# Kernel tuning notes

Hardware: AMD Instinct MI355X
Metric: run time of the kernel (lower is better)

The kernel has to match this reference:

```python
import jax, jax.numpy as jnp
import numpy as np

N, D, F, M, K = 4096, 1024, 4096, 2048, 307
EPS = 1e-5

def _ln(h, g, b):
    mu = jnp.mean(h, axis=-1, keepdims=True)
    var = jnp.mean(jnp.square(h - mu), axis=-1, keepdims=True)
    return (h - mu) * jax.lax.rsqrt(var + EPS) * g + b

def _attn(h, wq, wk, wv, mask):
    # wq/wk/wv stored as [D, D] so y = h @ w matches torch Linear(h) with W.T
    q = h @ wq
    k = h @ wk
    v = h @ wv
    s = (q @ k.T) * (1.0 / np.sqrt(D))  # [N, N]
    s = jnp.where(mask, -1e9, s)
    a = jax.nn.softmax(s, axis=-1)
    return a @ v, a

def _ffn(h, w1, b1, w2, b2):
    return jax.nn.gelu(h @ w1 + b1, approximate=False) @ w2 + b2

def setup_inputs() -> dict:
    ks = jax.random.split(jax.random.key(0), 32)
    s = 0.02
    p = lambda i, shape: (jax.random.normal(ks[i], shape, jnp.float32) * s)
    inp = {
        'x': jax.random.normal(ks[0], (N, D), jnp.float32),
        'real_edge_mask': jax.random.bernoulli(ks[1], 0.5, (N, N)),
        'fake_edge_mask': jax.random.bernoulli(ks[2], 0.5, (N, N)),
        'mask_nodes': jax.random.permutation(ks[3], N)[:M].astype(jnp.int32),
        'gene_idx': jnp.argsort(jax.random.uniform(ks[4], (M, D)), axis=-1)[:, :K].astype(jnp.int32),
        'wq1': p(5, (D, D)), 'wk1': p(6, (D, D)), 'wv1': p(7, (D, D)),
        'g1': jnp.ones((D,)), 'be1': jnp.zeros((D,)),
        'fw1': p(8, (D, F)), 'fb1': jnp.zeros((F,)),
        'fw2': p(9, (F, D)), 'fb2': jnp.zeros((D,)),
        'g2': jnp.ones((D,)), 'be2': jnp.zeros((D,)),
        'wq2': p(10, (D, D)), 'wk2': p(11, (D, D)), 'wv2': p(12, (D, D)),
        'g3': jnp.ones((D,)), 'be3': jnp.zeros((D,)),
        'hw1': p(13, (D, F)), 'hb1': jnp.zeros((F,)),
        'hw2': p(14, (F, D)), 'hb2': jnp.zeros((D,)),
        'g4': jnp.ones((D,)), 'be4': jnp.zeros((D,)),
        'head_w': p(15, (D, D)), 'head_b': jnp.zeros((D,)),
    }
    return inp

def reference(x, real_edge_mask, fake_edge_mask, mask_nodes, gene_idx,
              wq1, wk1, wv1, g1, be1, fw1, fb1, fw2, fb2, g2, be2,
              wq2, wk2, wv2, g3, be3, hw1, hb1, hw2, hb2, g4, be4,
              head_w, head_b):
    rows = jnp.arange(M)[:, None]  # [M, 1]
    # encoding_mask_nodes: zero K genes in each of M masked cells
    mask_x = x[mask_nodes].at[rows, gene_idx].set(0.0)
    use_x = x.at[mask_nodes].set(mask_x)

    hidden, encode_weights = _attn(use_x, wq1, wk1, wv1, real_edge_mask)
    hidden = _ln(hidden + use_x, g1, be1)
    hidden = _ln(hidden + _ffn(hidden, fw1, fb1, fw2, fb2), g2, be2)
    # NOTE: original `hidden[mask_nodes][gene_mask] = 0` is a no-op (copy), reproduced.

    recon, _decode_weights = _attn(hidden, wq2, wk2, wv2, real_edge_mask)
    recon = _ln(recon + hidden, g3, be3)
    recon = _ln(recon + _ffn(recon, hw1, hb1, hw2, hb2), g4, be4)
    h = recon @ head_w + head_b

    x_init = x[mask_nodes][rows, gene_idx]   # [M, K]
    x_recon = h[mask_nodes][rows, gene_idx]  # [M, K]
    return x_init, x_recon, encode_weights, recon
```

## Files before the change

### kernel.cpp

```cpp
#include <hip/hip_runtime.h>
#include <math.h>
#include <stdint.h>

typedef unsigned short u16;
typedef __attribute__((ext_vector_type(8))) short bf16x8;
typedef __attribute__((ext_vector_type(4))) float f32x4;

#define N_ 4096
#define D_ 1024
#define F_ 4096
#define M_ 2048
#define KG 307

__device__ __forceinline__ u16 f2bf(float f) {
  unsigned int u = __float_as_uint(f);
  unsigned int r = u + 0x7fffu + ((u >> 16) & 1u);
  return (u16)(r >> 16);
}

__device__ __forceinline__ float bf2f(u16 u) {
  return __uint_as_float((unsigned)u << 16);
}

__device__ __forceinline__ void gl_lds16(const u16* g, u16* l) {
  __builtin_amdgcn_global_load_lds(
      (__attribute__((address_space(1))) void*)(void*)g,
      (__attribute__((address_space(3))) void*)(void*)l,
      16, 0, 0);
}

enum { E_QKV = 0, E_SMASK = 1, E_PART = 2, E_GELU = 3 };
#define SMEM_BYTES 131072

template <int EPI>
__global__ __launch_bounds__(256, 4) void gemm128(
    const u16* __restrict__ A, const u16* __restrict__ B,
    void* __restrict__ C, void* __restrict__ C2,
    int Ndim, int Ksp, int lda, int ldb, long zstr,
    const float* __restrict__ bias) {
  __shared__ u16 As[2][128 * 32];
  __shared__ u16 Bs[2][128 * 32];
  const int tid = threadIdx.x;
  const int lane = tid & 63;
  const int wid = tid >> 6;
  const int wr = wid >> 1;
  const int wc = wid & 1;
  const int lr = lane & 15;
  const int lk = lane >> 4;

  const int gx = gridDim.x, gy = gridDim.y;
  const int bid = blockIdx.y * gx + blockIdx.x;
  const int bandM = gx >> 2, bandN = gy >> 1;
  const int xcd = bid & 7, ii = bid >> 3;
  const int mtile = (xcd >> 1) * bandM + ii / bandN;
  const int ntile = (xcd & 1) * bandN + ii % bandN;

  const long bm = (long)mtile * 128;
  const long bn = (long)ntile * 128;
  const long koff = (long)blockIdx.z * Ksp;

  f32x4 acc[4][4];
#pragma unroll
  for (int i = 0; i < 4; ++i)
#pragma unroll
    for (int j = 0; j < 4; ++j) acc[i][j] = f32x4{0.f, 0.f, 0.f, 0.f};

  auto stage = [&](int buf, long k0) {
#pragma unroll
    for (int i = 0; i < 2; ++i) {
      int o = tid + i * 256;
      int r = o >> 2, s = o & 3;
      gl_lds16(A + (bm + r) * (long)lda + k0 + ((s ^ ((r >> 1) & 3)) << 3), As[buf] + o * 8);
    }
#pragma unroll
    for (int i = 0; i < 2; ++i) {
      int o = tid + i * 256;
      int r = o >> 2, s = o & 3;
      gl_lds16(B + (bn + r) * (long)ldb + k0 + ((s ^ ((r >> 1) & 3)) << 3), Bs[buf] + o * 8);
    }
  };

  stage(0, koff);
  __syncthreads();
  const int nt = Ksp / 32;
  int cur = 0;
  for (int t = 0; t < nt; ++t) {
    if (t + 1 < nt) stage(cur ^ 1, koff + (long)(t + 1) * 32);
    bf16x8 av[4], bv[4];
#pragma unroll
    for (int mr = 0; mr < 4; ++mr) {
      int r = wr * 64 + mr * 16 + lr;
      av[mr] = *(const bf16x8*)(As[cur] + r * 32 + ((lk ^ ((r >> 1) & 3)) << 3));
    }
#pragma unroll
    for (int nr = 0; nr < 4; ++nr) {
      int r = wc * 64 + nr * 16 + lr;
      bv[nr] = *(const bf16x8*)(Bs[cur] + r * 32 + ((lk ^ ((r >> 1) & 3)) << 3));
    }
#pragma unroll
    for (int mr = 0; mr < 4; ++mr)
#pragma unroll
      for (int nr = 0; nr < 4; ++nr)
        acc[mr][nr] = __builtin_amdgcn_mfma_f32_16x16x32_bf16(av[mr], bv[nr], acc[mr][nr], 0, 0, 0);
    __syncthreads();
    cur ^= 1;
  }

  const bool z0 = (blockIdx.z == 0);
  float* Cz = (float*)C + (long)blockIdx.z * zstr;
#pragma unroll
  for (int mr = 0; mr < 4; ++mr) {
#pragma unroll
    for (int nr = 0; nr < 4; ++nr) {
#pragma unroll
      for (int j = 0; j < 4; ++j) {
        long row = bm + wr * 64 + mr * 16 + lk * 4 + j;
        long col = bn + wc * 64 + nr * 16 + lr;
        float v = acc[mr][nr][j];
        if constexpr (EPI == E_QKV) {
          if (col < 2048)
            ((u16*)C)[row * 2048 + col] = f2bf(v);
          else
            ((u16*)C2)[(col - 2048) * (long)N_ + row] = f2bf(v);
        } else if constexpr (EPI == E_PART) {
          Cz[row * Ndim + col] = v + ((z0 && bias) ? bias[col] : 0.f);
        }
      }
    }
  }
}

template <int EPI>
__global__ __launch_bounds__(512, 2) void gemm256(
    const u16* __restrict__ A, const u16* __restrict__ B,
    void* __restrict__ C, void* __restrict__ C2,
    int gridM, int gridN, int Ndim, int Ksp, int lda, int ldb, long zstr,
    const float* __restrict__ bias, const unsigned char* __restrict__ mask,
    float scale) {
  extern __shared__ __align__(16) char smem[];
  const int tid = threadIdx.x;
  const int lane = tid & 63;
  const int wid = tid >> 6;
  const int wr = wid >> 2;
  const int wc = wid & 3;
  const int lr = lane & 15;
  const int lk = lane >> 4;

  const int nwg = gridM * gridN;
  const int bid = blockIdx.x;
  const int q8 = nwg >> 3, r8 = nwg & 7;
  const int xcd = bid & 7, ii = bid >> 3;
  int wg = (xcd < r8 ? xcd * (q8 + 1) : r8 * (q8 + 1) + (xcd - r8) * q8) + ii;
  const int rowblk = wg / (gridN << 2);
  const int rem = wg - rowblk * (gridN << 2);
  const int mrem = gridM - (rowblk << 2);
  int mtile, ntile;
  if (mrem >= 4) {
    ntile = rem >> 2;
    mtile = (rowblk << 2) + (rem & 3);
  } else {
    ntile = rem / mrem;
    mtile = (rowblk << 2) + (rem - ntile * mrem);
  }
  const long bm = (long)mtile * 256;
  const long bn = (long)ntile * 256;
  const long koff = (long)blockIdx.y * Ksp;
  const int NT = Ksp >> 6;

  auto stA = [&](int t, int h) {
    char* base = smem + ((t & 1) << 15) + (h << 14);
    const long k0 = koff + ((long)t << 6);
#pragma unroll
    for (int j = 0; j < 2; ++j) {
      int o = tid + (j << 9);
      int r = o >> 3, s = o & 7;
      gl_lds16(A + (bm + (h << 7) + r) * (long)lda + k0 + ((s ^ (r & 7)) << 3),
               (u16*)(base + o * 16));
    }
  };
  auto stB = [&](int t, int h) {
    char* base = smem + 65536 + ((t & 1) << 15) + (h << 14);
    const long k0 = koff + ((long)t << 6);
#pragma unroll
    for (int j = 0; j < 2; ++j) {
      int o = tid + (j << 9);
      int r = o >> 3, s = o & 7;
      gl_lds16(B + (bn + (h << 7) + r) * (long)ldb + k0 + ((s ^ (r & 7)) << 3),
               (u16*)(base + o * 16));
    }
  };

  bf16x8 avA[2][2], avB[2][2], bv[4][2];
  f32x4 acc[8][4];
#pragma unroll
  for (int m = 0; m < 8; ++m)
#pragma unroll
    for (int n = 0; n < 4; ++n) acc[m][n] = f32x4{0.f, 0.f, 0.f, 0.f};

  auto rdAV = [&](bf16x8(&av)[2][2], const char* Ab_, int q) {
#pragma unroll
    for (int e = 0; e < 2; ++e)
#pragma unroll
      for (int ks = 0; ks < 2; ++ks) {
        int r = (wr << 7) + (q << 5) + (e << 4) + lr;
        av[e][ks] = *(const bf16x8*)(Ab_ + r * 128 + ((((ks << 2) | lk) ^ (r & 7)) << 4));
      }
  };
  auto rdBV = [&](const char* Bb_) {
#pragma unroll
    for (int n = 0; n < 4; ++n)
#pragma unroll
      for (int ks = 0; ks < 2; ++ks) {
        int r = (wc << 6) + (n << 4) + lr;
        bv[n][ks] = *(const bf16x8*)(Bb_ + r * 128 + ((((ks << 2) | lk) ^ (r & 7)) << 4));
      }
  };

#define MM(Q, AV)                                                              \
  __builtin_amdgcn_s_setprio(1);                                               \
  _Pragma("unroll") for (int e = 0; e < 2; ++e)                                \
  _Pragma("unroll") for (int n = 0; n < 4; ++n)                                \
  _Pragma("unroll") for (int ks = 0; ks < 2; ++ks)                             \
      acc[((Q) << 1) | e][n] = __builtin_amdgcn_mfma_f32_16x16x32_bf16(        \
          AV[e][ks], bv[n][ks], acc[((Q) << 1) | e][n], 0, 0, 0);              \
  __builtin_amdgcn_s_setprio(0);                                               \
  __builtin_amdgcn_sched_barrier(0);

  stA(0, 0);
  stA(0, 1);
  stB(0, 0);
  stB(0, 1);
  if (NT > 1) {
    stB(1, 0);
    stB(1, 1);
  }
  __builtin_amdgcn_sched_barrier(0);
  if (NT > 1)
    asm volatile("s_waitcnt vmcnt(4)");
  else
    asm volatile("s_waitcnt vmcnt(0)");
  __builtin_amdgcn_sched_barrier(0);
  __builtin_amdgcn_s_barrier();
  rdAV(avA, smem, 0);
  __builtin_amdgcn_sched_barrier(0);

  for (int t = 0; t < NT; ++t) {
    const char* Ab = smem + ((t & 1) << 15);
    const char* AbN = smem + (((t + 1) & 1) << 15);
    const char* Bb = smem + 65536 + ((t & 1) << 15);
    rdBV(Bb);
    rdAV(avB, Ab, 1);
    if (t + 1 < NT) stA(t + 1, 0);
    __builtin_amdgcn_sched_barrier(0);
    asm volatile("s_waitcnt lgkmcnt(4)");
    __builtin_amdgcn_sched_barrier(0);
    MM(0, avA)
    rdAV(avA, Ab, 2);
    if (t + 1 < NT) stA(t + 1, 1);
    __builtin_amdgcn_sched_barrier(0);
    asm volatile("s_waitcnt lgkmcnt(4)");
    __builtin_amdgcn_sched_barrier(0);
    MM(1, avB)
    __builtin_amdgcn_s_barrier();
    rdAV(avB, Ab, 3);
    if (t + 2 < NT) stB(t + 2, 0);
    __builtin_amdgcn_sched_barrier(0);
    asm volatile("s_waitcnt lgkmcnt(4)");
    __builtin_amdgcn_sched_barrier(0);
    MM(2, avA)
    asm volatile("s_waitcnt lgkmcnt(0)");
    if (t + 2 < NT)
      asm volatile("s_waitcnt vmcnt(2)");
    else
      asm volatile("s_waitcnt vmcnt(0)");
    __builtin_amdgcn_sched_barrier(0);
    __builtin_amdgcn_s_barrier();
    if (t + 1 < NT) rdAV(avA, AbN, 0);
    if (t + 2 < NT) stB(t + 2, 1);
    __builtin_amdgcn_sched_barrier(0);
    MM(3, avB)
  }
#undef MM

#pragma unroll
  for (int m = 0; m < 8; ++m) {
#pragma unroll
    for (int n = 0; n < 4; ++n) {
#pragma unroll
      for (int j = 0; j < 4; ++j) {
        long row = bm + (wr << 7) + (m << 4) + (lk << 2) + j;
        long col = bn + (wc << 6) + (n << 4) + lr;
        float v = acc[m][n][j];
        if constexpr (EPI == E_SMASK) {
          v *= scale;
          if (mask[row * Ndim + col]) v = -1e9f;
          ((u16*)C)[row * Ndim + col] = f2bf(v);
        } else if constexpr (EPI == E_GELU) {
          float tv = v + bias[col];
          float gl = 0.5f * tv * (1.0f + erff(tv * 0.70710678118654752f));
          ((u16*)C)[row * Ndim + col] = f2bf(gl);
        }
      }
    }
  }
}

__global__ __launch_bounds__(256) void tcvt3(const float* __restrict__ in0,
                                             const float* __restrict__ in1,
                                             const float* __restrict__ in2,
                                             u16* __restrict__ out, int R, int C) {
  __shared__ float tile[32][33];
  const float* in = (blockIdx.z == 0) ? in0 : (blockIdx.z == 1 ? in1 : in2);
  u16* dst = out + (size_t)blockIdx.z * R * C;
  int bx = blockIdx.x * 32;
  int by = blockIdx.y * 32;
  int tx = threadIdx.x & 31;
  int ty = threadIdx.x >> 5;
#pragma unroll
  for (int i = 0; i < 32; i += 8)
    tile[ty + i][tx] = in[(long)(by + ty + i) * C + bx + tx];
  __syncthreads();
#pragma unroll
  for (int i = 0; i < 32; i += 8)
    dst[(long)(bx + ty + i) * R + by + tx] = f2bf(tile[tx][ty + i]);
}

__global__ void copy_usex(const float* __restrict__ x, float* __restrict__ xf,
                          u16* __restrict__ xb, long n) {
  long i = (long)blockIdx.x * blockDim.x + threadIdx.x;
  if (i < n) {
    float v = x[i];
    xf[i] = v;
    xb[i] = f2bf(v);
  }
}

__global__ void mask_zero(const float* __restrict__ x, const int* __restrict__ mask_nodes,
                          const int* __restrict__ gene_idx, float* __restrict__ xf,
                          u16* __restrict__ xb, float* __restrict__ x_init) {
  int m = blockIdx.x;
  int k = threadIdx.x;
  if (k >= KG) return;
  int row = mask_nodes[m];
  int col = gene_idx[m * KG + k];
  x_init[m * KG + k] = x[(long)row * D_ + col];
  xf[(long)row * D_ + col] = 0.f;
  xb[(long)row * D_ + col] = 0;
}

template <int NY>
__global__ __launch_bounds__(256) void add_ln(const float* __restrict__ y, long ystr,
                                              const float* __restrict__ r,
                                              const float* __restrict__ g,
                                              const float* __restrict__ b,
                                              float* __restrict__ of, u16* __restrict__ ob) {
  int row = blockIdx.x;
  const float* yr = y + (long)row * D_;
  const float* rr = r + (long)row * D_;
  float v[4];
  float s = 0.f, ss = 0.f;
#pragma unroll
  for (int i = 0; i < 4; ++i) {
    int idx = threadIdx.x + i * 256;
    float t = rr[idx];
#pragma unroll
    for (int z = 0; z < NY; ++z) t += yr[z * ystr + idx];
    v[i] = t;
    s += t;
    ss += t * t;
  }
#pragma unroll
  for (int o = 32; o > 0; o >>= 1) {
    s += __shfl_down(s, o, 64);
    ss += __shfl_down(ss, o, 64);
  }
  __shared__ float red[8];
  int wid = threadIdx.x >> 6, lane = threadIdx.x & 63;
  if (lane == 0) {
    red[wid] = s;
    red[4 + wid] = ss;
  }
  __syncthreads();
  if (threadIdx.x == 0) {
    red[0] = red[0] + red[1] + red[2] + red[3];
    red[4] = red[4] + red[5] + red[6] + red[7];
  }
  __syncthreads();
  float mu = red[0] * (1.f / D_);
  float var = red[4] * (1.f / D_) - mu * mu;
  float rs = rsqrtf(var + 1e-5f);
#pragma unroll
  for (int i = 0; i < 4; ++i) {
    int idx = threadIdx.x + i * 256;
    float o = (v[i] - mu) * rs * g[idx] + b[idx];
    of[(long)row * D_ + idx] = o;
    ob[(long)row * D_ + idx] = f2bf(o);
  }
}

template <bool WF32>
__global__ __launch_bounds__(256) void softmax_row(const u16* __restrict__ sin,
                                                   float* __restrict__ a32,
                                                   u16* __restrict__ a16) {
  int row = blockIdx.x;
  const long base = (long)row * N_ + threadIdx.x * 16;
  const u16* sr = sin + base;
  float v[16];
  bf16x8 h0 = *(const bf16x8*)(sr);
  bf16x8 h1 = *(const bf16x8*)(sr + 8);
#pragma unroll
  for (int j = 0; j < 8; ++j) {
    v[j] = bf2f((u16)h0[j]);
    v[8 + j] = bf2f((u16)h1[j]);
  }
  float mx = v[0];
#pragma unroll
  for (int i = 1; i < 16; ++i) mx = fmaxf(mx, v[i]);
#pragma unroll
  for (int o = 32; o > 0; o >>= 1) mx = fmaxf(mx, __shfl_down(mx, o, 64));
  __shared__ float red[8];
  int wid = threadIdx.x >> 6, lane = threadIdx.x & 63;
  if (lane == 0) red[wid] = mx;
  __syncthreads();
  if (threadIdx.x == 0) red[0] = fmaxf(fmaxf(red[0], red[1]), fmaxf(red[2], red[3]));
  __syncthreads();
  mx = red[0];
  float sum = 0.f;
#pragma unroll
  for (int i = 0; i < 16; ++i) {
    v[i] = __expf(v[i] - mx);
    sum += v[i];
  }
#pragma unroll
  for (int o = 32; o > 0; o >>= 1) sum += __shfl_down(sum, o, 64);
  if (lane == 0) red[4 + wid] = sum;
  __syncthreads();
  if (threadIdx.x == 0) red[4] = red[4] + red[5] + red[6] + red[7];
  __syncthreads();
  float inv = 1.f / red[4];
  bf16x8 o0, o1;
#pragma unroll
  for (int j = 0; j < 8; ++j) {
    float p0 = v[j] * inv, p1 = v[8 + j] * inv;
    o0[j] = (short)f2bf(p0);
    o1[j] = (short)f2bf(p1);
    if constexpr (WF32) {
      a32[base + j] = p0;
      a32[base + 8 + j] = p1;
    }
  }
  *(bf16x8*)(a16 + base) = o0;
  *(bf16x8*)(a16 + base + 8) = o1;
}

__global__ void gather_rows(const u16* __restrict__ src, const int* __restrict__ mask_nodes,
                            u16* __restrict__ dst) {
  int m = blockIdx.x;
  int row = mask_nodes[m];
  for (int i = threadIdx.x; i < D_; i += 256)
    dst[(long)m * D_ + i] = src[(long)row * D_ + i];
}

__global__ void gather_recon(const float* __restrict__ h, const int* __restrict__ gene_idx,
                             float* __restrict__ xr) {
  int m = blockIdx.x;
  int k = threadIdx.x;
  if (k >= KG) return;
  xr[m * KG + k] = h[(long)m * D_ + gene_idx[m * KG + k]];
}

extern "C" void kernel_launch(void* const* d_in, const int* in_sizes, int n_in,
                              void* d_out, int out_size, void* d_ws, size_t ws_size,
                              hipStream_t stream) {
  const float* x = (const float*)d_in[0];
  const unsigned char* real_mask = (const unsigned char*)d_in[1];
  const int* mask_nodes = (const int*)d_in[3];
  const int* gene_idx = (const int*)d_in[4];
  const float* wq1 = (const float*)d_in[5];
  const float* wk1 = (const float*)d_in[6];
  const float* wv1 = (const float*)d_in[7];
  const float* g1 = (const float*)d_in[8];
  const float* be1 = (const float*)d_in[9];
  const float* fw1 = (const float*)d_in[10];
  const float* fb1 = (const float*)d_in[11];
  const float* fw2 = (const float*)d_in[12];
  const float* fb2 = (const float*)d_in[13];
  const float* g2 = (const float*)d_in[14];
  const float* be2 = (const float*)d_in[15];
  const float* wq2 = (const float*)d_in[16];
  const float* wk2 = (const float*)d_in[17];
  const float* wv2 = (const float*)d_in[18];
  const float* g3 = (const float*)d_in[19];
  const float* be3 = (const float*)d_in[20];
  const float* hw1 = (const float*)d_in[21];
  const float* hb1 = (const float*)d_in[22];
  const float* hw2 = (const float*)d_in[23];
  const float* hb2 = (const float*)d_in[24];
  const float* g4 = (const float*)d_in[25];
  const float* be4 = (const float*)d_in[26];
  const float* head_w = (const float*)d_in[27];
  const float* head_b = (const float*)d_in[28];

  float* out_xinit = (float*)d_out;
  float* out_xrecon = out_xinit + (long)M_ * KG;
  float* out_enc = out_xrecon + (long)M_ * KG;
  float* out_recon = out_enc + (long)N_ * N_;

  hipFuncSetAttribute((const void*)gemm256<E_SMASK>, hipFuncAttributeMaxDynamicSharedMemorySize, SMEM_BYTES);
  hipFuncSetAttribute((const void*)gemm256<E_GELU>, hipFuncAttributeMaxDynamicSharedMemorySize, SMEM_BYTES);

  char* w = (char*)d_ws;
  size_t off = 0;
  auto alloc = [&](size_t bytes) {
    void* p = w + off;
    off += (bytes + 255) & ~(size_t)255;
    return p;
  };
  float* useXf = (float*)alloc((size_t)N_ * D_ * 4);
  u16* useXb = (u16*)alloc((size_t)N_ * D_ * 2);
  u16* wslot = (u16*)alloc((size_t)D_ * F_ * 2);
  u16* qkb = (u16*)alloc((size_t)N_ * 2048 * 2);
  u16* vT = (u16*)alloc((size_t)D_ * N_ * 2);
  u16* tbuf = (u16*)alloc((size_t)N_ * F_ * 2);
  u16* aB = (u16*)alloc((size_t)N_ * N_ * 2);
  float* gout2 = (float*)alloc((size_t)2 * N_ * D_ * 4);
  float* actA = (float*)alloc((size_t)N_ * D_ * 4);
  float* actB = (float*)alloc((size_t)N_ * D_ * 4);
  u16* actB16 = (u16*)alloc((size_t)N_ * D_ * 2);
  u16* AgB = qkb;

  const float scale = 1.0f / 32.0f;
  const long nd = (long)N_ * D_;
  dim3 blk(256), blk5(512);

  copy_usex<<<dim3((unsigned)((nd + 255) / 256)), blk, 0, stream>>>(x, useXf, useXb, nd);
  mask_zero<<<dim3(M_), 320, 0, stream>>>(x, mask_nodes, gene_idx, useXf, useXb, out_xinit);

#define TCVT1(src, R, C, dst) \
  tcvt3<<<dim3((C) / 32, (R) / 32, 1), blk, 0, stream>>>(src, src, src, dst, R, C)
#define TCVTQ(s0, s1, s2, dst) \
  tcvt3<<<dim3(32, 32, 3), blk, 0, stream>>>(s0, s1, s2, dst, 1024, 1024)
#define G128(EP, GM, GN, Z, A, B, C, C2, ND, KS, LA, LB, ZS, BI) \
  gemm128<EP><<<dim3(GM, GN, Z), blk, 0, stream>>>(A, B, C, C2, ND, KS, LA, LB, ZS, BI)
#define G256(EP, GM, GN, A, B, C, ND, KS, LA, LB, BI, MK, SC)                                \
  gemm256<EP><<<dim3((GM) * (GN), 1), blk5, SMEM_BYTES, stream>>>(A, B, C, nullptr, GM, GN, \
                                                                  ND, KS, LA, LB, 0, BI, MK, SC)

  TCVTQ(wq1, wk1, wv1, wslot);
  G128(E_QKV, 32, 24, 1, useXb, wslot, qkb, vT, 3072, 1024, 1024, 1024, 0, nullptr);
  G256(E_SMASK, 16, 16, qkb, qkb + 1024, aB, 4096, 1024, 2048, 2048, nullptr, real_mask, scale);
  softmax_row<true><<<dim3(N_), blk, 0, stream>>>(aB, out_enc, aB);
  G128(E_PART, 32, 8, 2, aB, vT, gout2, nullptr, 1024, 2048, 4096, 4096, nd, nullptr);
  add_ln<2><<<dim3(N_), blk, 0, stream>>>(gout2, nd, useXf, g1, be1, actA, actB16);
  TCVT1(fw1, D_, F_, wslot);
  G256(E_GELU, 16, 16, actB16, wslot, tbuf, 4096, 1024, 1024, 1024, fb1, nullptr, 0.f);
  TCVT1(fw2, F_, D_, wslot);
  G128(E_PART, 32, 8, 2, tbuf, wslot, gout2, nullptr, 1024, 2048, 4096, 4096, nd, fb2);
  add_ln<2><<<dim3(N_), blk, 0, stream>>>(gout2, nd, actA, g2, be2, actB, actB16);

  TCVTQ(wq2, wk2, wv2, wslot);
  G128(E_QKV, 32, 24, 1, actB16, wslot, qkb, vT, 3072, 1024, 1024, 1024, 0, nullptr);
  G256(E_SMASK, 16, 16, qkb, qkb + 1024, aB, 4096, 1024, 2048, 2048, nullptr, real_mask, scale);
  softmax_row<false><<<dim3(N_), blk, 0, stream>>>(aB, nullptr, aB);
  G128(E_PART, 32, 8, 2, aB, vT, gout2, nullptr, 1024, 2048, 4096, 4096, nd, nullptr);
  add_ln<2><<<dim3(N_), blk, 0, stream>>>(gout2, nd, actB, g3, be3, actA, actB16);
  TCVT1(hw1, D_, F_, wslot);
  G256(E_GELU, 16, 16, actB16, wslot, tbuf, 4096, 1024, 1024, 1024, hb1, nullptr, 0.f);
  TCVT1(hw2, F_, D_, wslot);
  G128(E_PART, 32, 8, 2, tbuf, wslot, gout2, nullptr, 1024, 2048, 4096, 4096, nd, hb2);
  add_ln<2><<<dim3(N_), blk, 0, stream>>>(gout2, nd, actA, g4, be4, out_recon, actB16);

  gather_rows<<<dim3(M_), blk, 0, stream>>>(actB16, mask_nodes, AgB);
  TCVT1(head_w, D_, D_, wslot);
  G128(E_PART, 16, 8, 1, AgB, wslot, gout2, nullptr, 1024, 1024, 1024, 1024, 0, head_b);
  gather_recon<<<dim3(M_), 320, 0, stream>>>(gout2, gene_idx, out_xrecon);
#undef TCVT1
#undef TCVTQ
#undef G128
#undef G256
}
```

Baseline: 682.4 us.

## Replace split-K GEMMs with 128x64-tile full-K GEMM kernel for N=1024 outputs

Adds a gemm64 kernel with 128x64 output tiles that loops over the full K=4096 instead of splitting K in two with 128x128 tiles. This targets the four attention-value and FFN-down GEMMs, and lets add_ln read a single partial buffer instead of summing two. It drops the extra fp32 partial write/read traffic and gives the same 512-block grid. The cost is smaller tiles with less operand reuse per block.

```diff
diff --git a/kernel.cpp b/kernel.cpp
--- a/kernel.cpp
+++ b/kernel.cpp
@@ -31,6 +31,84 @@
 
 enum { E_QKV = 0, E_SMASK = 1, E_PART = 2, E_GELU = 3 };
 #define SMEM_BYTES 131072
+
+__global__ __launch_bounds__(256, 4) void gemm64(
+    const u16* __restrict__ A, const u16* __restrict__ B, float* __restrict__ C,
+    int Ndim, int K, int lda, int ldb, const float* __restrict__ bias) {
+  __shared__ u16 As[2][128 * 32];
+  __shared__ u16 Bs[2][64 * 32];
+  const int tid = threadIdx.x;
+  const int lane = tid & 63;
+  const int wv = tid >> 6;
+  const int lr = lane & 15;
+  const int lk = lane >> 4;
+
+  const int gx = gridDim.x, gy = gridDim.y;
+  const int bid = blockIdx.y * gx + blockIdx.x;
+  const int bandM = gx >> 2, bandN = gy >> 1;
+  const int xcd = bid & 7, ii = bid >> 3;
+  const int mtile = (xcd >> 1) * bandM + ii / bandN;
+  const int ntile = (xcd & 1) * bandN + ii % bandN;
+  const long bm = (long)mtile * 128;
+  const long bn = (long)ntile * 64;
+
+  f32x4 acc[2][4];
+#pragma unroll
+  for (int i = 0; i < 2; ++i)
+#pragma unroll
+    for (int j = 0; j < 4; ++j) acc[i][j] = f32x4{0.f, 0.f, 0.f, 0.f};
+
+  auto stage = [&](int buf, long k0) {
+#pragma unroll
+    for (int i = 0; i < 2; ++i) {
+      int o = tid + i * 256;
+      int r = o >> 2, s = o & 3;
+      gl_lds16(A + (bm + r) * (long)lda + k0 + ((s ^ ((r >> 1) & 3)) << 3), As[buf] + o * 8);
+    }
+    {
+      int o = tid;
+      int r = o >> 2, s = o & 3;
+      gl_lds16(B + (bn + r) * (long)ldb + k0 + ((s ^ ((r >> 1) & 3)) << 3), Bs[buf] + o * 8);
+    }
+  };
+
+  stage(0, 0);
+  __syncthreads();
+  const int nt = K / 32;
+  int cur = 0;
+  for (int t = 0; t < nt; ++t) {
+    if (t + 1 < nt) stage(cur ^ 1, (long)(t + 1) * 32);
+    bf16x8 av[2], bv[4];
+#pragma unroll
+    for (int mr = 0; mr < 2; ++mr) {
+      int r = wv * 32 + mr * 16 + lr;
+      av[mr] = *(const bf16x8*)(As[cur] + r * 32 + ((lk ^ ((r >> 1) & 3)) << 3));
+    }
+#pragma unroll
+    for (int nr = 0; nr < 4; ++nr) {
+      int r = nr * 16 + lr;
+      bv[nr] = *(const bf16x8*)(Bs[cur] + r * 32 + ((lk ^ ((r >> 1) & 3)) << 3));
+    }
+#pragma unroll
+    for (int mr = 0; mr < 2; ++mr)
+#pragma unroll
+      for (int nr = 0; nr < 4; ++nr)
+        acc[mr][nr] = __builtin_amdgcn_mfma_f32_16x16x32_bf16(av[mr], bv[nr], acc[mr][nr], 0, 0, 0);
+    __syncthreads();
+    cur ^= 1;
+  }
+
+#pragma unroll
+  for (int mr = 0; mr < 2; ++mr)
+#pragma unroll
+    for (int nr = 0; nr < 4; ++nr)
+#pragma unroll
+      for (int j = 0; j < 4; ++j) {
+        long row = bm + wv * 32 + mr * 16 + lk * 4 + j;
+        long col = bn + nr * 16 + lr;
+        C[row * Ndim + col] = acc[mr][nr][j] + (bias ? bias[col] : 0.f);
+      }
+}
 
 template <int EPI>
 __global__ __launch_bounds__(256, 4) void gemm128(
@@ -523,7 +601,7 @@
   u16* vT = (u16*)alloc((size_t)D_ * N_ * 2);
   u16* tbuf = (u16*)alloc((size_t)N_ * F_ * 2);
   u16* aB = (u16*)alloc((size_t)N_ * N_ * 2);
-  float* gout2 = (float*)alloc((size_t)2 * N_ * D_ * 4);
+  float* gout = (float*)alloc((size_t)N_ * D_ * 4);
   float* actA = (float*)alloc((size_t)N_ * D_ * 4);
   float* actB = (float*)alloc((size_t)N_ * D_ * 4);
   u16* actB16 = (u16*)alloc((size_t)N_ * D_ * 2);
@@ -542,6 +620,8 @@
   tcvt3<<<dim3(32, 32, 3), blk, 0, stream>>>(s0, s1, s2, dst, 1024, 1024)
 #define G128(EP, GM, GN, Z, A, B, C, C2, ND, KS, LA, LB, ZS, BI) \
   gemm128<EP><<<dim3(GM, GN, Z), blk, 0, stream>>>(A, B, C, C2, ND, KS, LA, LB, ZS, BI)
+#define G64(A, B, C, ND, K, LA, LB, BI) \
+  gemm64<<<dim3(32, 16), blk, 0, stream>>>(A, B, C, ND, K, LA, LB, BI)
 #define G256(EP, GM, GN, A, B, C, ND, KS, LA, LB, BI, MK, SC)                                \
   gemm256<EP><<<dim3((GM) * (GN), 1), blk5, SMEM_BYTES, stream>>>(A, B, C, nullptr, GM, GN, \
                                                                   ND, KS, LA, LB, 0, BI, MK, SC)
@@ -550,32 +630,33 @@
   G128(E_QKV, 32, 24, 1, useXb, wslot, qkb, vT, 3072, 1024, 1024, 1024, 0, nullptr);
   G256(E_SMASK, 16, 16, qkb, qkb + 1024, aB, 4096, 1024, 2048, 2048, nullptr, real_mask, scale);
   softmax_row<true><<<dim3(N_), blk, 0, stream>>>(aB, out_enc, aB);
-  G128(E_PART, 32, 8, 2, aB, vT, gout2, nullptr, 1024, 2048, 4096, 4096, nd, nullptr);
-  add_ln<2><<<dim3(N_), blk, 0, stream>>>(gout2, nd, useXf, g1, be1, actA, actB16);
+  G64(aB, vT, gout, 1024, 4096, 4096, 4096, nullptr);
+  add_ln<1><<<dim3(N_), blk, 0, stream>>>(gout, 0, useXf, g1, be1, actA, actB16);
   TCVT1(fw1, D_, F_, wslot);
   G256(E_GELU, 16, 16, actB16, wslot, tbuf, 4096, 1024, 1024, 1024, fb1, nullptr, 0.f);
   TCVT1(fw2, F_, D_, wslot);
-  G128(E_PART, 32, 8, 2, tbuf, wslot, gout2, nullptr, 1024, 2048, 4096, 4096, nd, fb2);
-  add_ln<2><<<dim3(N_), blk, 0, stream>>>(gout2, nd, actA, g2, be2, actB, actB16);
+  G64(tbuf, wslot, gout, 1024, 4096, 4096, 4096, fb2);
+  add_ln<1><<<dim3(N_), blk, 0, stream>>>(gout, 0, actA, g2, be2, actB, actB16);
 
   TCVTQ(wq2, wk2, wv2, wslot);
   G128(E_QKV, 32, 24, 1, actB16, wslot, qkb, vT, 3072, 1024, 1024, 1024, 0, nullptr);
   G256(E_SMASK, 16, 16, qkb, qkb + 1024, aB, 4096, 1024, 2048, 2048, nullptr, real_mask, scale);
   softmax_row<false><<<dim3(N_), blk, 0, stream>>>(aB, nullptr, aB);
-  G128(E_PART, 32, 8, 2, aB, vT, gout2, nullptr, 1024, 2048, 4096, 4096, nd, nullptr);
-  add_ln<2><<<dim3(N_), blk, 0, stream>>>(gout2, nd, actB, g3, be3, actA, actB16);
+  G64(aB, vT, gout, 1024, 4096, 4096, 4096, nullptr);
+  add_ln<1><<<dim3(N_), blk, 0, stream>>>(gout, 0, actB, g3, be3, actA, actB16);
   TCVT1(hw1, D_, F_, wslot);
   G256(E_GELU, 16, 16, actB16, wslot, tbuf, 4096, 1024, 1024, 1024, hb1, nullptr, 0.f);
   TCVT1(hw2, F_, D_, wslot);
-  G128(E_PART, 32, 8, 2, tbuf, wslot, gout2, nullptr, 1024, 2048, 4096, 4096, nd, hb2);
-  add_ln<2><<<dim3(N_), blk, 0, stream>>>(gout2, nd, actA, g4, be4, out_recon, actB16);
+  G64(tbuf, wslot, gout, 1024, 4096, 4096, 4096, hb2);
+  add_ln<1><<<dim3(N_), blk, 0, stream>>>(gout, 0, actA, g4, be4, out_recon, actB16);
 
   gather_rows<<<dim3(M_), blk, 0, stream>>>(actB16, mask_nodes, AgB);
   TCVT1(head_w, D_, D_, wslot);
-  G128(E_PART, 16, 8, 1, AgB, wslot, gout2, nullptr, 1024, 1024, 1024, 1024, 0, head_b);
-  gather_recon<<<dim3(M_), 320, 0, stream>>>(gout2, gene_idx, out_xrecon);
+  G128(E_PART, 16, 8, 1, AgB, wslot, gout, nullptr, 1024, 1024, 1024, 1024, 0, head_b);
+  gather_recon<<<dim3(M_), 320, 0, stream>>>(gout, gene_idx, out_xrecon);
 #undef TCVT1
 #undef TCVTQ
 #undef G128
+#undef G64
 #undef G256
 }
```

Result: slower. 727.9 us (+6.7%).
